# Kernel optimization log

Hardware: AMD Instinct MI355X
Metric: run time of the kernel (lower is better)

The kernel has to match this reference:

```python
import jax, jax.numpy as jnp
import numpy as np

B, F, D = 8192, 1024, 128  # batch, agent input feats, latent (Bernoulli) size


def setup_inputs() -> dict:
    key = jax.random.key(0)
    kx, kw = jax.random.split(key)
    x = jax.random.normal(kx, (B, F), dtype=jnp.float32)
    # scale so logits land in a non-degenerate range around [0,1]
    W = jax.random.normal(kw, (F, D), dtype=jnp.float32) * (1.0 / np.sqrt(F))
    b = jnp.zeros((D,), dtype=jnp.float32)
    return {"x": x, "W": W, "b": b}


def reference(x, W, b):
    """SparseMAPWrapper.forward with a linear agent, budget=0 (bernoulli_smap).

    SparseMAP over independent Bernoullis: mu* = clip(theta, 0, 1); the sparse
    distribution over bit-vector configurations is the nested-threshold
    decomposition of mu* (support <= D+1), padded with zero-weight rows.
    """
    theta = x @ W + b                      # [B, D] logits from the agent
    mu = jnp.clip(theta, 0.0, 1.0)         # SparseMAP marginals
    u = -jnp.sort(-mu, axis=-1)            # [B, D] descending
    # configs c_j = 1[mu >= u_j]; prepend the all-zeros configuration
    configs = (mu[:, None, :] >= u[:, :, None]).astype(theta.dtype)  # [B, D, D]
    zero_cfg = jnp.zeros((mu.shape[0], 1, mu.shape[1]), dtype=theta.dtype)
    sample = jnp.concatenate([zero_cfg, configs], axis=1)            # [B, D+1, D]
    # weights: w0 = 1 - u_1 (all-zeros), w_j = u_j - u_{j+1}, u_{D+1} = 0
    u_next = jnp.concatenate([u[:, 1:], jnp.zeros_like(u[:, :1])], axis=1)
    distr = jnp.concatenate([1.0 - u[:, :1], u - u_next], axis=1)    # [B, D+1]
    pos = distr > 0
    safe = jnp.where(pos, distr, 1.0)
    entropy_distr = jnp.sum(jnp.where(pos, -distr * jnp.log(safe), 0.0))
    entropy_distr = entropy_distr / distr.shape[0]
    support = jnp.sum(pos, axis=-1)        # [B] per-sample support sizes
    return sample, distr, entropy_distr, support
```

## Files before the change

kernel.cpp:

```cpp
#include <hip/hip_runtime.h>
#include <hip/hip_bf16.h>
#include <math.h>

#define BATCH 8192
#define FEAT  1024
#define DLAT  128
#define DP1   129

typedef float f32x4 __attribute__((ext_vector_type(4)));

#define TILE_M 16
#define KT     32
#define NK0    (FEAT / KT)

__global__ __launch_bounds__(256) void gemm_theta(
    const float* __restrict__ x, const float* __restrict__ W,
    const float* __restrict__ b, float* __restrict__ theta) {
  __shared__ __align__(16) float xs[2][TILE_M][KT];
  __shared__ __align__(16) float wsh[2][KT][DLAT];
  const int row0 = blockIdx.x * TILE_M;
  const int t = threadIdx.x;
  const int c4 = (t & 31) * 4;
  const int r2 = (t >> 5) * 2;

  const int lxr = t >> 3;
  const int lxc = (t & 7) * 4;
  float acc[2][4] = {{0.f}};

  {
    if (t < 128)
      *(float4*)&xs[0][lxr][lxc] =
          *(const float4*)(x + (size_t)(row0 + lxr) * FEAT + lxc);
    #pragma unroll
    for (int i = 0; i < 4; ++i) {
      const int idx = t + i * 256;
      const int kk  = idx >> 5;
      const int cq  = (idx & 31) * 4;
      *(float4*)&wsh[0][kk][cq] = *(const float4*)(W + (size_t)kk * DLAT + cq);
    }
  }
  __syncthreads();

  int buf = 0;
  for (int k0it = 0; k0it < NK0; ++k0it) {
    float4 px;
    float4 pw[4];
    const bool hasNext = (k0it + 1 < NK0);
    if (hasNext) {
      const int k0n = (k0it + 1) * KT;
      if (t < 128)
        px = *(const float4*)(x + (size_t)(row0 + lxr) * FEAT + k0n + lxc);
      #pragma unroll
      for (int i = 0; i < 4; ++i) {
        const int idx = t + i * 256;
        const int kk  = idx >> 5;
        const int cq  = (idx & 31) * 4;
        pw[i] = *(const float4*)(W + (size_t)(k0n + kk) * DLAT + cq);
      }
    }

    #pragma unroll
    for (int kk = 0; kk < KT; kk += 4) {
      float4 xv[2], wv[4];
      #pragma unroll
      for (int r = 0; r < 2; ++r) xv[r] = *(const float4*)&xs[buf][r2 + r][kk];
      #pragma unroll
      for (int i = 0; i < 4; ++i) wv[i] = *(const float4*)&wsh[buf][kk + i][c4];
      #pragma unroll
      for (int r = 0; r < 2; ++r) {
        const float* xr = (const float*)&xv[r];
        #pragma unroll
        for (int i = 0; i < 4; ++i) {
          const float* wc = (const float*)&wv[i];
          #pragma unroll
          for (int c = 0; c < 4; ++c)
            acc[r][c] = fmaf(xr[i], wc[c], acc[r][c]);
        }
      }
    }

    if (hasNext) {
      if (t < 128) *(float4*)&xs[buf ^ 1][lxr][lxc] = px;
      #pragma unroll
      for (int i = 0; i < 4; ++i) {
        const int idx = t + i * 256;
        const int kk  = idx >> 5;
        const int cq  = (idx & 31) * 4;
        *(float4*)&wsh[buf ^ 1][kk][cq] = pw[i];
      }
    }
    __syncthreads();
    buf ^= 1;
  }

  const float4 bv = *(const float4*)(b + c4);
  #pragma unroll
  for (int r = 0; r < 2; ++r) {
    float4 o;
    o.x = acc[r][0] + bv.x;
    o.y = acc[r][1] + bv.y;
    o.z = acc[r][2] + bv.z;
    o.w = acc[r][3] + bv.w;
    *(float4*)(theta + (size_t)(row0 + r2 + r) * DLAT + c4) = o;
  }
}

__global__ __launch_bounds__(256) void smap_rows(
    const float* __restrict__ theta, float* __restrict__ sample,
    float* __restrict__ distr, float* __restrict__ support,
    float* __restrict__ entpart) {
  __shared__ __align__(16) float mu[DLAT];
  __shared__ __align__(16) float s[DLAT];
  __shared__ float entw[4];
  __shared__ int   posw[4];
  const int row = blockIdx.x;
  const int t = threadIdx.x;

  if (t < DLAT) {
    float v = theta[(size_t)row * DLAT + t];
    v = fminf(fmaxf(v, 0.0f), 1.0f);
    mu[t] = v;
  }
  __syncthreads();

  if (t < DLAT) {
    const float v = mu[t];
    int rank = 0;
    #pragma unroll
    for (int q = 0; q < DLAT / 4; ++q) {
      const float4 m4 = *(const float4*)&mu[q * 4];
      rank += (m4.x > v || (m4.x == v && (q * 4 + 0) < t)) ? 1 : 0;
      rank += (m4.y > v || (m4.y == v && (q * 4 + 1) < t)) ? 1 : 0;
      rank += (m4.z > v || (m4.z == v && (q * 4 + 2) < t)) ? 1 : 0;
      rank += (m4.w > v || (m4.w == v && (q * 4 + 3) < t)) ? 1 : 0;
    }
    s[rank] = v;
  }
  __syncthreads();

  {
    const int jl = t >> 5;
    const int cq = (t & 31) * 4;
    f32x4* out = (f32x4*)(sample + (size_t)row * DP1 * DLAT);
    const float4 m4 = *(const float4*)&mu[cq];
    #pragma unroll
    for (int it = 0; it < 16; ++it) {
      const int j = it * 8 + jl;
      const float thr = (j == 0) ? 2.0f : s[j - 1];
      f32x4 o;
      o.x = (m4.x >= thr) ? 1.0f : 0.0f;
      o.y = (m4.y >= thr) ? 1.0f : 0.0f;
      o.z = (m4.z >= thr) ? 1.0f : 0.0f;
      o.w = (m4.w >= thr) ? 1.0f : 0.0f;
      __builtin_nontemporal_store(o, &out[(size_t)j * (DLAT / 4) + (cq >> 2)]);
    }
    if (jl == 0) {
      const float thr = s[DLAT - 1];
      f32x4 o;
      o.x = (m4.x >= thr) ? 1.0f : 0.0f;
      o.y = (m4.y >= thr) ? 1.0f : 0.0f;
      o.z = (m4.z >= thr) ? 1.0f : 0.0f;
      o.w = (m4.w >= thr) ? 1.0f : 0.0f;
      __builtin_nontemporal_store(o, &out[(size_t)DLAT * (DLAT / 4) + (cq >> 2)]);
    }
  }

  float w = 0.0f; int pos = 0; float ent = 0.0f;
  if (t < DP1) {
    if (t == 0)          w = 1.0f - s[0];
    else if (t < DLAT)   w = s[t - 1] - s[t];
    else                 w = s[DLAT - 1];
    __builtin_nontemporal_store(w, &distr[(size_t)row * DP1 + t]);
    if (w > 0.0f) { pos = 1; ent = -w * logf(w); }
  }
  #pragma unroll
  for (int off = 32; off > 0; off >>= 1) {
    ent += __shfl_xor(ent, off, 64);
    pos += __shfl_xor(pos, off, 64);
  }
  if ((t & 63) == 0) { entw[t >> 6] = ent; posw[t >> 6] = pos; }
  __syncthreads();
  if (t == 0) {
    entpart[row] = (entw[0] + entw[1]) + (entw[2] + entw[3]);
    support[row] = (float)(posw[0] + posw[1] + posw[2] + posw[3]);
  }
}

__global__ __launch_bounds__(1024) void reduce_ent(
    const float* __restrict__ entpart, float* __restrict__ outent) {
  __shared__ double red[1024];
  const int t = threadIdx.x;
  double acc = 0.0;
  for (int i = t; i < BATCH; i += 1024) acc += (double)entpart[i];
  red[t] = acc;
  __syncthreads();
  for (int off = 512; off > 0; off >>= 1) {
    if (t < off) red[t] += red[t + off];
    __syncthreads();
  }
  if (t == 0) *outent = (float)(red[0] / (double)BATCH);
}

extern "C" void kernel_launch(void* const* d_in, const int* in_sizes, int n_in,
                              void* d_out, int out_size, void* d_ws, size_t ws_size,
                              hipStream_t stream) {
  const float* x = (const float*)d_in[0];
  const float* W = (const float*)d_in[1];
  const float* b = (const float*)d_in[2];

  float* out = (float*)d_out;
  const size_t n_sample = (size_t)BATCH * DP1 * DLAT;
  const size_t n_distr  = (size_t)BATCH * DP1;
  float* sample  = out;
  float* distr   = out + n_sample;
  float* entropy = out + n_sample + n_distr;
  float* support = out + n_sample + n_distr + 1;

  float* theta   = (float*)d_ws;
  float* entpart = theta + (size_t)BATCH * DLAT;

  gemm_theta<<<BATCH / TILE_M, 256, 0, stream>>>(x, W, b, theta);
  smap_rows<<<BATCH, 256, 0, stream>>>(theta, sample, distr, support, entpart);
  reduce_ent<<<1, 1024, 0, stream>>>(entpart, entropy);
}
```

Measured before the change: 644.7 us.

## Fuse GEMM and SparseMAP row processing into one kernel per 16-row tile

After: 684.2 us. +6.1%, slower.

```diff
diff --git a/kernel.cpp b/kernel.cpp
--- a/kernel.cpp
+++ b/kernel.cpp
@@ -6,23 +6,29 @@
 #define FEAT  1024
 #define DLAT  128
 #define DP1   129
-
-typedef float f32x4 __attribute__((ext_vector_type(4)));
-
 #define TILE_M 16
 #define KT     32
 #define NK0    (FEAT / KT)
-
-__global__ __launch_bounds__(256) void gemm_theta(
+#define NBLK   (BATCH / TILE_M)
+
+typedef float f32x4 __attribute__((ext_vector_type(4)));
+
+__global__ __launch_bounds__(256) void fused_smap(
     const float* __restrict__ x, const float* __restrict__ W,
-    const float* __restrict__ b, float* __restrict__ theta) {
+    const float* __restrict__ b, float* __restrict__ sample,
+    float* __restrict__ distr, float* __restrict__ support,
+    float* __restrict__ entpart) {
   __shared__ __align__(16) float xs[2][TILE_M][KT];
   __shared__ __align__(16) float wsh[2][KT][DLAT];
+  __shared__ __align__(16) float mu[TILE_M][DLAT + 4];
+  __shared__ __align__(16) float ss[TILE_M][DLAT + 4];
+  __shared__ int   poscnt[TILE_M];
+  __shared__ float entw[4];
+
   const int row0 = blockIdx.x * TILE_M;
   const int t = threadIdx.x;
   const int c4 = (t & 31) * 4;
   const int r2 = (t >> 5) * 2;
-
   const int lxr = t >> 3;
   const int lxc = (t & 7) * 4;
   float acc[2][4] = {{0.f}};
@@ -39,6 +45,7 @@
       *(float4*)&wsh[0][kk][cq] = *(const float4*)(W + (size_t)kk * DLAT + cq);
     }
   }
+  if (t < TILE_M) poscnt[t] = 0;
   __syncthreads();
 
   int buf = 0;
@@ -58,7 +65,6 @@
         pw[i] = *(const float4*)(W + (size_t)(k0n + kk) * DLAT + cq);
       }
     }
-
     #pragma unroll
     for (int kk = 0; kk < KT; kk += 4) {
       float4 xv[2], wv[4];
@@ -78,7 +84,6 @@
         }
       }
     }
-
     if (hasNext) {
       if (t < 128) *(float4*)&xs[buf ^ 1][lxr][lxc] = px;
       #pragma unroll
@@ -93,108 +98,97 @@
     buf ^= 1;
   }
 
-  const float4 bv = *(const float4*)(b + c4);
-  #pragma unroll
-  for (int r = 0; r < 2; ++r) {
-    float4 o;
-    o.x = acc[r][0] + bv.x;
-    o.y = acc[r][1] + bv.y;
-    o.z = acc[r][2] + bv.z;
-    o.w = acc[r][3] + bv.w;
-    *(float4*)(theta + (size_t)(row0 + r2 + r) * DLAT + c4) = o;
-  }
-}
-
-__global__ __launch_bounds__(256) void smap_rows(
-    const float* __restrict__ theta, float* __restrict__ sample,
-    float* __restrict__ distr, float* __restrict__ support,
-    float* __restrict__ entpart) {
-  __shared__ __align__(16) float mu[DLAT];
-  __shared__ __align__(16) float s[DLAT];
-  __shared__ float entw[4];
-  __shared__ int   posw[4];
-  const int row = blockIdx.x;
-  const int t = threadIdx.x;
-
-  if (t < DLAT) {
-    float v = theta[(size_t)row * DLAT + t];
-    v = fminf(fmaxf(v, 0.0f), 1.0f);
-    mu[t] = v;
-  }
-  __syncthreads();
-
-  if (t < DLAT) {
-    const float v = mu[t];
-    int rank = 0;
-    #pragma unroll
+  {
+    const float4 bv = *(const float4*)(b + c4);
+    #pragma unroll
+    for (int r = 0; r < 2; ++r) {
+      float4 o;
+      o.x = fminf(fmaxf(acc[r][0] + bv.x, 0.0f), 1.0f);
+      o.y = fminf(fmaxf(acc[r][1] + bv.y, 0.0f), 1.0f);
+      o.z = fminf(fmaxf(acc[r][2] + bv.z, 0.0f), 1.0f);
+      o.w = fminf(fmaxf(acc[r][3] + bv.w, 0.0f), 1.0f);
+      *(float4*)&mu[r2 + r][c4] = o;
+    }
+  }
+  __syncthreads();
+
+  {
+    const int srow = t >> 4;
+    const int e0   = (t & 15) * 8;
+    float vloc[8]; int rk[8];
+    #pragma unroll
+    for (int e = 0; e < 8; ++e) { vloc[e] = mu[srow][e0 + e]; rk[e] = 0; }
     for (int q = 0; q < DLAT / 4; ++q) {
-      const float4 m4 = *(const float4*)&mu[q * 4];
-      rank += (m4.x > v || (m4.x == v && (q * 4 + 0) < t)) ? 1 : 0;
-      rank += (m4.y > v || (m4.y == v && (q * 4 + 1) < t)) ? 1 : 0;
-      rank += (m4.z > v || (m4.z == v && (q * 4 + 2) < t)) ? 1 : 0;
-      rank += (m4.w > v || (m4.w == v && (q * 4 + 3) < t)) ? 1 : 0;
-    }
-    s[rank] = v;
+      const float4 m4 = *(const float4*)&mu[srow][q * 4];
+      #pragma unroll
+      for (int e = 0; e < 8; ++e) {
+        const float v = vloc[e]; const int gi = e0 + e;
+        rk[e] += (m4.x > v || (m4.x == v && (q * 4 + 0) < gi)) ? 1 : 0;
+        rk[e] += (m4.y > v || (m4.y == v && (q * 4 + 1) < gi)) ? 1 : 0;
+        rk[e] += (m4.z > v || (m4.z == v && (q * 4 + 2) < gi)) ? 1 : 0;
+        rk[e] += (m4.w > v || (m4.w == v && (q * 4 + 3) < gi)) ? 1 : 0;
+      }
+    }
+    #pragma unroll
+    for (int e = 0; e < 8; ++e) ss[srow][rk[e]] = vloc[e];
   }
   __syncthreads();
 
   {
     const int jl = t >> 5;
     const int cq = (t & 31) * 4;
-    f32x4* out = (f32x4*)(sample + (size_t)row * DP1 * DLAT);
-    const float4 m4 = *(const float4*)&mu[cq];
-    #pragma unroll
-    for (int it = 0; it < 16; ++it) {
-      const int j = it * 8 + jl;
-      const float thr = (j == 0) ? 2.0f : s[j - 1];
-      f32x4 o;
-      o.x = (m4.x >= thr) ? 1.0f : 0.0f;
-      o.y = (m4.y >= thr) ? 1.0f : 0.0f;
-      o.z = (m4.z >= thr) ? 1.0f : 0.0f;
-      o.w = (m4.w >= thr) ? 1.0f : 0.0f;
-      __builtin_nontemporal_store(o, &out[(size_t)j * (DLAT / 4) + (cq >> 2)]);
-    }
-    if (jl == 0) {
-      const float thr = s[DLAT - 1];
-      f32x4 o;
-      o.x = (m4.x >= thr) ? 1.0f : 0.0f;
-      o.y = (m4.y >= thr) ? 1.0f : 0.0f;
-      o.z = (m4.z >= thr) ? 1.0f : 0.0f;
-      o.w = (m4.w >= thr) ? 1.0f : 0.0f;
-      __builtin_nontemporal_store(o, &out[(size_t)DLAT * (DLAT / 4) + (cq >> 2)]);
-    }
-  }
-
-  float w = 0.0f; int pos = 0; float ent = 0.0f;
-  if (t < DP1) {
-    if (t == 0)          w = 1.0f - s[0];
-    else if (t < DLAT)   w = s[t - 1] - s[t];
-    else                 w = s[DLAT - 1];
-    __builtin_nontemporal_store(w, &distr[(size_t)row * DP1 + t]);
-    if (w > 0.0f) { pos = 1; ent = -w * logf(w); }
+    for (int r = 0; r < TILE_M; ++r) {
+      f32x4* outp = (f32x4*)(sample + (size_t)(row0 + r) * DP1 * DLAT);
+      const float4 m4 = *(const float4*)&mu[r][cq];
+      #pragma unroll
+      for (int it = 0; it < 16; ++it) {
+        const int j = it * 8 + jl;
+        const float thr = (j == 0) ? 2.0f : ss[r][j - 1];
+        f32x4 o;
+        o.x = (m4.x >= thr) ? 1.0f : 0.0f;
+        o.y = (m4.y >= thr) ? 1.0f : 0.0f;
+        o.z = (m4.z >= thr) ? 1.0f : 0.0f;
+        o.w = (m4.w >= thr) ? 1.0f : 0.0f;
+        __builtin_nontemporal_store(o, &outp[(size_t)j * (DLAT / 4) + (cq >> 2)]);
+      }
+      if (jl == 0) {
+        const float thr = ss[r][DLAT - 1];
+        f32x4 o;
+        o.x = (m4.x >= thr) ? 1.0f : 0.0f;
+        o.y = (m4.y >= thr) ? 1.0f : 0.0f;
+        o.z = (m4.z >= thr) ? 1.0f : 0.0f;
+        o.w = (m4.w >= thr) ? 1.0f : 0.0f;
+        __builtin_nontemporal_store(o, &outp[(size_t)DLAT * (DLAT / 4) + (cq >> 2)]);
+      }
+    }
+  }
+
+  float ent = 0.0f;
+  for (int item = t; item < TILE_M * DP1; item += 256) {
+    const int r = item / DP1;
+    const int j = item - r * DP1;
+    float w;
+    if (j == 0)          w = 1.0f - ss[r][0];
+    else if (j < DLAT)   w = ss[r][j - 1] - ss[r][j];
+    else                 w = ss[r][DLAT - 1];
+    __builtin_nontemporal_store(w, &distr[(size_t)(row0 + r) * DP1 + j]);
+    if (w > 0.0f) { atomicAdd(&poscnt[r], 1); ent += -w * logf(w); }
   }
   #pragma unroll
-  for (int off = 32; off > 0; off >>= 1) {
-    ent += __shfl_xor(ent, off, 64);
-    pos += __shfl_xor(pos, off, 64);
-  }
-  if ((t & 63) == 0) { entw[t >> 6] = ent; posw[t >> 6] = pos; }
-  __syncthreads();
-  if (t == 0) {
-    entpart[row] = (entw[0] + entw[1]) + (entw[2] + entw[3]);
-    support[row] = (float)(posw[0] + posw[1] + posw[2] + posw[3]);
-  }
+  for (int off = 32; off > 0; off >>= 1) ent += __shfl_xor(ent, off, 64);
+  if ((t & 63) == 0) entw[t >> 6] = ent;
+  __syncthreads();
+  if (t < TILE_M) support[row0 + t] = (float)poscnt[t];
+  if (t == 0) entpart[blockIdx.x] = (entw[0] + entw[1]) + (entw[2] + entw[3]);
 }
 
-__global__ __launch_bounds__(1024) void reduce_ent(
+__global__ __launch_bounds__(512) void reduce_ent(
     const float* __restrict__ entpart, float* __restrict__ outent) {
-  __shared__ double red[1024];
+  __shared__ double red[512];
   const int t = threadIdx.x;
-  double acc = 0.0;
-  for (int i = t; i < BATCH; i += 1024) acc += (double)entpart[i];
-  red[t] = acc;
-  __syncthreads();
-  for (int off = 512; off > 0; off >>= 1) {
+  red[t] = (double)entpart[t];
+  __syncthreads();
+  for (int off = 256; off > 0; off >>= 1) {
     if (t < off) red[t] += red[t + off];
     __syncthreads();
   }
@@ -216,10 +210,8 @@
   float* entropy = out + n_sample + n_distr;
   float* support = out + n_sample + n_distr + 1;
 
-  float* theta   = (float*)d_ws;
-  float* entpart = theta + (size_t)BATCH * DLAT;
-
-  gemm_theta<<<BATCH / TILE_M, 256, 0, stream>>>(x, W, b, theta);
-  smap_rows<<<BATCH, 256, 0, stream>>>(theta, sample, distr, support, entpart);
-  reduce_ent<<<1, 1024, 0, stream>>>(entpart, entropy);
+  float* entpart = (float*)d_ws;
+
+  fused_smap<<<NBLK, 256, 0, stream>>>(x, W, b, sample, distr, support, entpart);
+  reduce_ent<<<1, 512, 0, stream>>>(entpart, entropy);
 }
```
